# Kernel tuning notes

Hardware: AMD Instinct MI355X
Metric: run time of the kernel (lower is better)

Reference implementation:

```python
import jax, jax.numpy as jnp
import numpy as np


def setup_inputs() -> dict:
    key = jax.random.key(0)
    kq, kk, kv = jax.random.split(key, 3)
    B, H, T, D = 1, 16, 4096, 64
    Q = jax.random.normal(kq, (B, H, T, D), dtype=jnp.float32)
    K = jax.random.normal(kk, (B, H, T, D), dtype=jnp.float32)
    V = jax.random.normal(kv, (B, H, T, D), dtype=jnp.float32)
    return {"Q": Q, "K": K, "V": V}


def reference(Q, K, V):
    B, H, T, D = Q.shape
    # ALiBi slopes: m_h = 2^(-8*h/H), h = 1..H (deterministic buffer)
    slopes = jnp.exp2(-8.0 * jnp.arange(1, H + 1, dtype=jnp.float32) / H)
    pos = jnp.arange(T, dtype=jnp.float32)
    dist = jnp.abs(pos[None, :] - pos[:, None])          # (T, T)
    bias = slopes[:, None, None] * dist                   # (H, T, T)
    scale = jnp.sqrt(jnp.asarray(D, dtype=Q.dtype))
    scores = jnp.einsum('bhtd,bhsd->bhts', Q, K) / scale - bias[None]
    attn = jax.nn.softmax(scores, axis=-1)
    return jnp.einsum('bhts,bhsd->bhtd', attn, V)
```

## Files before the change

kernel.cpp:

```cpp
#include <hip/hip_runtime.h>
#include <hip/hip_bf16.h>
#include <stdint.h>

typedef float f4    __attribute__((ext_vector_type(4)));
typedef float f32x4 __attribute__((ext_vector_type(4)));
typedef short s16x8 __attribute__((ext_vector_type(8)));
typedef short s16x4 __attribute__((ext_vector_type(4)));
typedef unsigned short u16;

#define T_LEN 4096
#define NHEAD 16
#define DHEAD 64
#define KVBLK 64
#define NT    (T_LEN / KVBLK)

#if __has_builtin(__builtin_amdgcn_exp2f)
#define EXP2(x) __builtin_amdgcn_exp2f(x)
#else
#define EXP2(x) exp2f(x)
#endif

#define SLOT_F 4160
#define CONV_BYTES ((size_t)16777216)
#define SLOTS_BAL  2304
#define BAL_BYTES  (CONV_BYTES + (size_t)SLOTS_BAL * SLOT_F * 4u)

__device__ __constant__ int NCARR[8] = {2,3,4,4,5,6,6,6};
__device__ __constant__ int SBARR[8] = {0,128,320,576,832,1152,1536,1920};

__device__ __forceinline__ uint32_t pk2(float a, float b){
  uint32_t ua = __builtin_bit_cast(uint32_t, a) + 0x8000u;
  uint32_t ub = __builtin_bit_cast(uint32_t, b) + 0x8000u;
  return __builtin_amdgcn_perm(ub, ua, 0x07060302u);
}
__device__ __forceinline__ int swk(int r){ return (r ^ (r >> 3)) & 7; }
__device__ __forceinline__ int sw(int r){ return swk(r) << 3; }

__global__ __launch_bounds__(256)
void cvt_kv(const float* __restrict__ K, const float* __restrict__ V,
            u16* __restrict__ Kb, u16* __restrict__ VT){
  __shared__ u16 tile[64][66];
  if (blockIdx.x < 2048){
    const size_t i = ((size_t)blockIdx.x * 256 + threadIdx.x) * 8;
    f4 a = *(const f4*)(K + i);
    f4 b = *(const f4*)(K + i + 4);
    union { uint32_t w[4]; s16x8 v; } u;
    u.w[0] = pk2(a[0], a[1]); u.w[1] = pk2(a[2], a[3]);
    u.w[2] = pk2(b[0], b[1]); u.w[3] = pk2(b[2], b[3]);
    *(s16x8*)(Kb + i) = u.v;
  } else {
    const int vb = blockIdx.x - 2048;
    const int h  = vb >> 6;
    const int kt = vb & 63;
    const int t  = threadIdx.x;
    const float* Vh = V + ((size_t)h * T_LEN + kt * 64) * DHEAD;

    const int r = t >> 2, c = (t & 3) * 16;
    f4 x0 = *(const f4*)(Vh + r*64 + c);
    f4 x1 = *(const f4*)(Vh + r*64 + c + 4);
    f4 x2 = *(const f4*)(Vh + r*64 + c + 8);
    f4 x3 = *(const f4*)(Vh + r*64 + c + 12);
    uint32_t* tp = (uint32_t*)&tile[r][c];
    tp[0] = pk2(x0[0],x0[1]); tp[1] = pk2(x0[2],x0[3]);
    tp[2] = pk2(x1[0],x1[1]); tp[3] = pk2(x1[2],x1[3]);
    tp[4] = pk2(x2[0],x2[1]); tp[5] = pk2(x2[2],x2[3]);
    tp[6] = pk2(x3[0],x3[1]); tp[7] = pk2(x3[2],x3[3]);
    __syncthreads();

    const int d = t >> 2, ks = (t & 3) * 16;
    u16* op = VT + ((size_t)h * DHEAD + d) * T_LEN + kt * 64 + ks;
    union { uint32_t w[4]; s16x8 v; } o0, o1;
#pragma unroll
    for (int q = 0; q < 4; ++q)
      o0.w[q] = (uint32_t)tile[ks + 2*q][d]     | ((uint32_t)tile[ks + 2*q + 1][d] << 16);
#pragma unroll
    for (int q = 0; q < 4; ++q)
      o1.w[q] = (uint32_t)tile[ks + 8 + 2*q][d] | ((uint32_t)tile[ks + 9 + 2*q][d] << 16);
    *(s16x8*)(op)     = o0.v;
    *(s16x8*)(op + 8) = o1.v;
  }
}

__global__ __launch_bounds__(256, 4)
void alibi_attn5(const float* __restrict__ Qg,
                 const u16* __restrict__ Kb,
                 const u16* __restrict__ VTb,
                 float* __restrict__ Og,
                 float* __restrict__ part)
{
  __shared__ u16 kbuf[2][KVBLK * DHEAD];
  __shared__ u16 vbuf[2][DHEAD * KVBLK];

  int h, qt, c, n;
  {
    int r = blockIdx.x;
    if (r < 1152){
      h = 15 - r / 384; r %= 384; n = 6; qt = r / 6; c = r % 6;
    } else if ((r -= 1152) < 320){
      h = 12; n = 5; qt = r / 5; c = r % 5;
    } else if ((r -= 320) < 512){
      h = 11 - (r >> 8); r &= 255; n = 4; qt = r >> 2; c = r & 3;
    } else if ((r -= 512) < 192){
      h = 9; n = 3; qt = r / 3; c = r % 3;
    } else if ((r -= 192) < 128){
      h = 8; n = 2; qt = r >> 1; c = r & 1;
    } else {
      r -= 128; h = r >> 6; qt = r & 63; n = 1; c = 0;
    }
  }

  const int tid  = threadIdx.x;
  const int wv   = tid >> 6;
  const int lane = tid & 63;
  const int lg   = lane >> 4;
  const int ln   = lane & 15;

  const int q0   = qt * 64;
  const int qrow = q0 + wv * 16 + ln;
  const float slope = exp2f(-0.5f * (float)(h + 1));
  const float cs = 0.125f * 1.44269504089f;
  const float bs = slope * 1.44269504089f;
  const size_t headoff = (size_t)h * T_LEN * DHEAD;

  const int Di = (int)(36.0f / bs);
  int lo = (q0 - Di) >> 6;           if (lo < 0) lo = 0;
  int hi = (q0 + 63 + Di) >> 6;      if (hi > NT - 1) hi = NT - 1;
  const int len = hi - lo + 1;
  const int start = lo + (c * len) / n;
  const int end   = lo + ((c + 1) * len) / n;

  s16x8 qf0, qf1;
  {
    const float* qp = Qg + headoff + (size_t)qrow * DHEAD + lg * 8;
    f4 x = *(const f4*)qp;        f4 y = *(const f4*)(qp + 4);
    f4 z = *(const f4*)(qp + 32); f4 v = *(const f4*)(qp + 36);
    union { uint32_t w_[4]; s16x8 v_; } u0, u1;
    u0.w_[0] = pk2(x[0]*cs, x[1]*cs); u0.w_[1] = pk2(x[2]*cs, x[3]*cs);
    u0.w_[2] = pk2(y[0]*cs, y[1]*cs); u0.w_[3] = pk2(y[2]*cs, y[3]*cs);
    u1.w_[0] = pk2(z[0]*cs, z[1]*cs); u1.w_[1] = pk2(z[2]*cs, z[3]*cs);
    u1.w_[2] = pk2(v[0]*cs, v[1]*cs); u1.w_[3] = pk2(v[2]*cs, v[3]*cs);
    qf0 = u0.v_; qf1 = u1.v_;
  }

  f32x4 acc[4];
#pragma unroll
  for (int dt = 0; dt < 4; ++dt) acc[dt] = (f32x4)(0.0f);
  float lsum = 0.0f;
  const float base0 = (float)qrow - (float)(lg * 4);

  int koffs[4][2];
#pragma unroll
  for (int kt = 0; kt < 4; ++kt){
    const int key = kt*16 + ln, sz = sw(key);
    koffs[kt][0] = (((key*64      + lg*8) ^ sz)) * 2;
    koffs[kt][1] = (((key*64 + 32 + lg*8) ^ sz)) * 2;
  }
  int voffs[4][4];
#pragma unroll
  for (int dt = 0; dt < 4; ++dt){
    const int d = dt*16 + ln, sz = sw(d);
#pragma unroll
    for (int kt = 0; kt < 4; ++kt)
      voffs[dt][kt] = (((d*64 + kt*16 + lg*4) ^ sz)) * 2;
  }

  const u16* Kh = Kb  + headoff;
  const u16* Vh = VTb + headoff;
  const int sA = wv * 128 + lane;
  const int sB = sA + 64;
  const int keyA = sA >> 3, gA = (sA & 7) ^ swk(keyA);
  const int keyB = sB >> 3, gB = (sB & 7) ^ swk(keyB);
  const int kidxA = keyA * 64 + gA * 8;
  const int kidxB = keyB * 64 + gB * 8;
  const int vidxA = keyA * T_LEN + gA * 8;
  const int vidxB = keyB * T_LEN + gB * 8;
  const int dstA = sA * 16, dstB = sB * 16;

  s16x8 rkA, rkB, rvA, rvB;
  auto ldregs = [&](int t){
    const u16* kp = Kh + (size_t)t * (KVBLK * DHEAD);
    const u16* vp = Vh + (size_t)t * KVBLK;
    rkA = *(const s16x8*)(kp + kidxA);  rkB = *(const s16x8*)(kp + kidxB);
    rvA = *(const s16x8*)(vp + vidxA);  rvB = *(const s16x8*)(vp + vidxB);
  };
  auto wrregs = [&](u16* kb_, u16* vb_){
    *(s16x8*)((char*)kb_ + dstA) = rkA;  *(s16x8*)((char*)kb_ + dstB) = rkB;
    *(s16x8*)((char*)vb_ + dstA) = rvA;  *(s16x8*)((char*)vb_ + dstB) = rvB;
  };

  auto compute = [&](const u16* kb_, const u16* vb_, int kv){
    f32x4 S[4];
    __builtin_amdgcn_s_setprio(1);
#pragma unroll
    for (int kt = 0; kt < 4; ++kt){
      s16x8 k0 = *(const s16x8*)((const char*)kb_ + koffs[kt][0]);
      s16x8 k1 = *(const s16x8*)((const char*)kb_ + koffs[kt][1]);
      f32x4 cc = (f32x4)(0.0f);
      cc = __builtin_amdgcn_mfma_f32_16x16x32_bf16(k0, qf0, cc, 0, 0, 0);
      cc = __builtin_amdgcn_mfma_f32_16x16x32_bf16(k1, qf1, cc, 0, 0, 0);
      S[kt] = cc;
    }
    __builtin_amdgcn_s_setprio(0);

    const float bi = base0 - (float)(kv * KVBLK);
    float p[16];
#pragma unroll
    for (int kt = 0; kt < 4; ++kt)
#pragma unroll
      for (int r = 0; r < 4; ++r)
        p[kt*4 + r] = EXP2(fmaf(-bs, fabsf(bi - (float)(kt*16 + r)), S[kt][r]));

    lsum += (((p[0]+p[1]) + (p[2]+p[3])) + ((p[4]+p[5]) + (p[6]+p[7])))
          + (((p[8]+p[9]) + (p[10]+p[11])) + ((p[12]+p[13]) + (p[14]+p[15])));

    s16x4 pb[4];
#pragma unroll
    for (int kt = 0; kt < 4; ++kt){
      union { uint32_t w_[2]; s16x4 v_; } u;
      u.w_[0] = pk2(p[kt*4+0], p[kt*4+1]);
      u.w_[1] = pk2(p[kt*4+2], p[kt*4+3]);
      pb[kt] = u.v_;
    }

    __builtin_amdgcn_s_setprio(1);
#pragma unroll
    for (int dt = 0; dt < 4; ++dt){
#pragma unroll
      for (int kt = 0; kt < 4; ++kt){
        const s16x4 vf = *(const s16x4*)((const char*)vb_ + voffs[dt][kt]);
        acc[dt] = __builtin_amdgcn_mfma_f32_16x16x16bf16_1k(vf, pb[kt], acc[dt], 0, 0, 0);
      }
    }
    __builtin_amdgcn_s_setprio(0);
  };

  {
    ldregs(start);
    wrregs(kbuf[0], vbuf[0]);
    __syncthreads();

    const int hi_i = end - 1;
    int t = start;
#pragma unroll 1
    while (t + 1 < hi_i){
      ldregs(t + 1);
      compute(kbuf[0], vbuf[0], t);
      wrregs(kbuf[1], vbuf[1]);
      __syncthreads();
      ldregs(t + 2);
      compute(kbuf[1], vbuf[1], t + 1);
      wrregs(kbuf[0], vbuf[0]);
      __syncthreads();
      t += 2;
    }
    if (t < hi_i){
      ldregs(t + 1);
      compute(kbuf[0], vbuf[0], t);
      wrregs(kbuf[1], vbuf[1]);
      __syncthreads();
      compute(kbuf[1], vbuf[1], t + 1);
    } else {
      compute(kbuf[0], vbuf[0], t);
    }
  }

  lsum += __shfl_xor(lsum, 16, 64);
  lsum += __shfl_xor(lsum, 32, 64);

  if (n == 1){
    const float inv = 1.0f / lsum;
    float* op = Og + headoff + (size_t)qrow * DHEAD + lg * 4;
#pragma unroll
    for (int dt = 0; dt < 4; ++dt){
      f4 o;
      o[0] = acc[dt][0] * inv; o[1] = acc[dt][1] * inv;
      o[2] = acc[dt][2] * inv; o[3] = acc[dt][3] * inv;
      *(f4*)(op + dt*16) = o;
    }
  } else {
    float* slot = part + (size_t)(SBARR[h - 8] + qt * n + c) * SLOT_F;
    const int row = wv * 16 + ln;
    float* op = slot + row * 64 + lg * 4;
#pragma unroll
    for (int dt = 0; dt < 4; ++dt)
      *(f4*)(op + dt*16) = acc[dt];
    if (lg == 0) slot[4096 + row] = lsum;
  }
}

__global__ __launch_bounds__(256)
void combine_k(const float* __restrict__ part, float* __restrict__ Og){
  const int h  = 8 + (blockIdx.x >> 6);
  const int qt = blockIdx.x & 63;
  const int n  = NCARR[h - 8];
  const int sb = SBARR[h - 8] + qt * n;

  const int t   = threadIdx.x;
  const int row = t >> 2;
  const int seg = (t & 3) * 16;

  f4 a0 = (f4)(0.0f), a1 = (f4)(0.0f), a2 = (f4)(0.0f), a3 = (f4)(0.0f);
  float l = 0.0f;
#pragma unroll 1
  for (int c = 0; c < n; ++c){
    const float* sp = part + (size_t)(sb + c) * SLOT_F;
    const float* rp = sp + row * 64 + seg;
    a0 += *(const f4*)(rp);
    a1 += *(const f4*)(rp + 4);
    a2 += *(const f4*)(rp + 8);
    a3 += *(const f4*)(rp + 12);
    l  += sp[4096 + row];
  }
  const float inv = 1.0f / l;
  float* op = Og + (((size_t)h * T_LEN + qt * 64 + row) * DHEAD) + seg;
  f4 o0, o1, o2, o3;
  o0[0]=a0[0]*inv; o0[1]=a0[1]*inv; o0[2]=a0[2]*inv; o0[3]=a0[3]*inv;
  o1[0]=a1[0]*inv; o1[1]=a1[1]*inv; o1[2]=a1[2]*inv; o1[3]=a1[3]*inv;
  o2[0]=a2[0]*inv; o2[1]=a2[1]*inv; o2[2]=a2[2]*inv; o2[3]=a2[3]*inv;
  o3[0]=a3[0]*inv; o3[1]=a3[1]*inv; o3[2]=a3[2]*inv; o3[3]=a3[3]*inv;
  *(f4*)(op)      = o0;
  *(f4*)(op + 4)  = o1;
  *(f4*)(op + 8)  = o2;
  *(f4*)(op + 12) = o3;
}

__global__ __launch_bounds__(256, 4)
void alibi_attn4(const float* __restrict__ Qg,
                 const u16* __restrict__ Kb,
                 const u16* __restrict__ VTb,
                 float* __restrict__ Og)
{
  __shared__ u16 kbuf[2][KVBLK * DHEAD];
  __shared__ u16 vbuf[2][DHEAD * KVBLK];

  const int bid = blockIdx.x;
  const int fid = (bid & 7) * 128 + (bid >> 3);
  const int h  = fid & 15;
  const int qt = fid >> 4;

  const int tid  = threadIdx.x;
  const int wv   = tid >> 6;
  const int lane = tid & 63;
  const int lg   = lane >> 4;
  const int ln   = lane & 15;

  const int q0   = qt * 64;
  const int qrow = q0 + wv * 16 + ln;
  const float slope = exp2f(-0.5f * (float)(h + 1));
  const float cs = 0.125f * 1.44269504089f;
  const float bs = slope * 1.44269504089f;
  const size_t headoff = (size_t)h * T_LEN * DHEAD;

  const int Di = (int)(36.0f / bs);
  int lo = (q0 - Di) >> 6;           if (lo < 0) lo = 0;
  int hi = (q0 + 63 + Di) >> 6;      if (hi > NT - 1) hi = NT - 1;

  s16x8 qf0, qf1;
  {
    const float* qp = Qg + headoff + (size_t)qrow * DHEAD + lg * 8;
    f4 x = *(const f4*)qp;        f4 y = *(const f4*)(qp + 4);
    f4 z = *(const f4*)(qp + 32); f4 v = *(const f4*)(qp + 36);
    union { uint32_t w_[4]; s16x8 v_; } u0, u1;
    u0.w_[0] = pk2(x[0]*cs, x[1]*cs); u0.w_[1] = pk2(x[2]*cs, x[3]*cs);
    u0.w_[2] = pk2(y[0]*cs, y[1]*cs); u0.w_[3] = pk2(y[2]*cs, y[3]*cs);
    u1.w_[0] = pk2(z[0]*cs, z[1]*cs); u1.w_[1] = pk2(z[2]*cs, z[3]*cs);
    u1.w_[2] = pk2(v[0]*cs, v[1]*cs); u1.w_[3] = pk2(v[2]*cs, v[3]*cs);
    qf0 = u0.v_; qf1 = u1.v_;
  }

  f32x4 acc[4];
#pragma unroll
  for (int dt = 0; dt < 4; ++dt) acc[dt] = (f32x4)(0.0f);
  float lsum = 0.0f;
  const float base0 = (float)qrow - (float)(lg * 4);

  int koffs[4][2];
#pragma unroll
  for (int kt = 0; kt < 4; ++kt){
    const int key = kt*16 + ln, sz = sw(key);
    koffs[kt][0] = (((key*64      + lg*8) ^ sz)) * 2;
    koffs[kt][1] = (((key*64 + 32 + lg*8) ^ sz)) * 2;
  }
  int voffs[4][4];
#pragma unroll
  for (int dt = 0; dt < 4; ++dt){
    const int d = dt*16 + ln, sz = sw(d);
#pragma unroll
    for (int kt = 0; kt < 4; ++kt)
      voffs[dt][kt] = (((d*64 + kt*16 + lg*4) ^ sz)) * 2;
  }

  const u16* Kh = Kb  + headoff;
  const u16* Vh = VTb + headoff;
  const int sA = wv * 128 + lane;
  const int sB = sA + 64;
  const int keyA = sA >> 3, gA = (sA & 7) ^ swk(keyA);
  const int keyB = sB >> 3, gB = (sB & 7) ^ swk(keyB);
  const int kidxA = keyA * 64 + gA * 8;
  const int kidxB = keyB * 64 + gB * 8;
  const int vidxA = keyA * T_LEN + gA * 8;
  const int vidxB = keyB * T_LEN + gB * 8;
  const int dstA = sA * 16, dstB = sB * 16;

  s16x8 rkA, rkB, rvA, rvB;
  auto ldregs = [&](int t){
    const u16* kp = Kh + (size_t)t * (KVBLK * DHEAD);
    const u16* vp = Vh + (size_t)t * KVBLK;
    rkA = *(const s16x8*)(kp + kidxA);  rkB = *(const s16x8*)(kp + kidxB);
    rvA = *(const s16x8*)(vp + vidxA);  rvB = *(const s16x8*)(vp + vidxB);
  };
  auto wrregs = [&](u16* kb_, u16* vb_){
    *(s16x8*)((char*)kb_ + dstA) = rkA;  *(s16x8*)((char*)kb_ + dstB) = rkB;
    *(s16x8*)((char*)vb_ + dstA) = rvA;  *(s16x8*)((char*)vb_ + dstB) = rvB;
  };

  auto compute = [&](const u16* kb_, const u16* vb_, int kv){
    f32x4 S[4];
    __builtin_amdgcn_s_setprio(1);
#pragma unroll
    for (int kt = 0; kt < 4; ++kt){
      s16x8 k0 = *(const s16x8*)((const char*)kb_ + koffs[kt][0]);
      s16x8 k1 = *(const s16x8*)((const char*)kb_ + koffs[kt][1]);
      f32x4 cc = (f32x4)(0.0f);
      cc = __builtin_amdgcn_mfma_f32_16x16x32_bf16(k0, qf0, cc, 0, 0, 0);
      cc = __builtin_amdgcn_mfma_f32_16x16x32_bf16(k1, qf1, cc, 0, 0, 0);
      S[kt] = cc;
    }
    __builtin_amdgcn_s_setprio(0);

    const float bi = base0 - (float)(kv * KVBLK);
    float p[16];
#pragma unroll
    for (int kt = 0; kt < 4; ++kt)
#pragma unroll
      for (int r = 0; r < 4; ++r)
        p[kt*4 + r] = EXP2(fmaf(-bs, fabsf(bi - (float)(kt*16 + r)), S[kt][r]));

    lsum += (((p[0]+p[1]) + (p[2]+p[3])) + ((p[4]+p[5]) + (p[6]+p[7])))
          + (((p[8]+p[9]) + (p[10]+p[11])) + ((p[12]+p[13]) + (p[14]+p[15])));

    s16x4 pb[4];
#pragma unroll
    for (int kt = 0; kt < 4; ++kt){
      union { uint32_t w_[2]; s16x4 v_; } u;
      u.w_[0] = pk2(p[kt*4+0], p[kt*4+1]);
      u.w_[1] = pk2(p[kt*4+2], p[kt*4+3]);
      pb[kt] = u.v_;
    }

    __builtin_amdgcn_s_setprio(1);
#pragma unroll
    for (int dt = 0; dt < 4; ++dt){
#pragma unroll
      for (int kt = 0; kt < 4; ++kt){
        const s16x4 vf = *(const s16x4*)((const char*)vb_ + voffs[dt][kt]);
        acc[dt] = __builtin_amdgcn_mfma_f32_16x16x16bf16_1k(vf, pb[kt], acc[dt], 0, 0, 0);
      }
    }
    __builtin_amdgcn_s_setprio(0);
  };

  ldregs(lo);
  wrregs(kbuf[0], vbuf[0]);
  __syncthreads();

  int t = lo;
#pragma unroll 1
  while (t + 1 < hi){
    ldregs(t + 1);
    compute(kbuf[0], vbuf[0], t);
    wrregs(kbuf[1], vbuf[1]);
    __syncthreads();
    ldregs(t + 2);
    compute(kbuf[1], vbuf[1], t + 1);
    wrregs(kbuf[0], vbuf[0]);
    __syncthreads();
    t += 2;
  }
  if (t < hi){
    ldregs(t + 1);
    compute(kbuf[0], vbuf[0], t);
    wrregs(kbuf[1], vbuf[1]);
    __syncthreads();
    compute(kbuf[1], vbuf[1], t + 1);
  } else {
    compute(kbuf[0], vbuf[0], t);
  }

  lsum += __shfl_xor(lsum, 16, 64);
  lsum += __shfl_xor(lsum, 32, 64);
  const float inv = 1.0f / lsum;
  float* op = Og + headoff + (size_t)qrow * DHEAD + lg * 4;
#pragma unroll
  for (int dt = 0; dt < 4; ++dt){
    f4 o;
    o[0] = acc[dt][0] * inv; o[1] = acc[dt][1] * inv;
    o[2] = acc[dt][2] * inv; o[3] = acc[dt][3] * inv;
    *(f4*)(op + dt*16) = o;
  }
}

__global__ __launch_bounds__(256, 2)
void alibi_attn_fb(const float* __restrict__ Qg,
                   const float* __restrict__ Kg,
                   const float* __restrict__ Vg,
                   float* __restrict__ Og)
{
  __shared__ u16 kbuf[2][KVBLK * DHEAD];
  __shared__ u16 vbuf[2][DHEAD * KVBLK];

  const int bid = blockIdx.x;
  const int fid = (bid & 7) * 64 + (bid >> 3);
  const int h  = fid >> 5;
  const int qt = fid & 31;

  const int tid  = threadIdx.x;
  const int wave = tid >> 6;
  const int lane = tid & 63;
  const int lg   = lane >> 4;
  const int ln   = lane & 15;

  const int qb = qt * 128 + wave * 32;
  const float slope = exp2f(-0.5f * (float)(h + 1));
  const float cs = 0.125f * 1.44269504089f;
  const float bs = slope * 1.44269504089f;
  const size_t headoff = (size_t)h * T_LEN * DHEAD;

  s16x8 qf[2][2];
#pragma unroll
  for (int rg = 0; rg < 2; ++rg)
#pragma unroll
    for (int dh = 0; dh < 2; ++dh){
      const float* qp = Qg + headoff + (size_t)(qb + rg*16 + ln) * DHEAD + dh*32 + lg*8;
      f4 x = *(const f4*)qp;
      f4 y = *(const f4*)(qp + 4);
      union { uint32_t w[4]; s16x8 v; } u;
      u.w[0] = pk2(x[0]*cs, x[1]*cs);
      u.w[1] = pk2(x[2]*cs, x[3]*cs);
      u.w[2] = pk2(y[0]*cs, y[1]*cs);
      u.w[3] = pk2(y[2]*cs, y[3]*cs);
      qf[rg][dh] = u.v;
    }

  f32x4 acc[2][4];
#pragma unroll
  for (int rg = 0; rg < 2; ++rg)
#pragma unroll
    for (int dt = 0; dt < 4; ++dt) acc[rg][dt] = (f32x4)(0.0f);
  float mreg[2] = {-1e30f, -1e30f};
  float lreg[2] = {0.0f, 0.0f};
  const float qposf[2] = {(float)(qb + ln), (float)(qb + 16 + ln)};
  const float koffb = (float)(lg * 4);

  f4 st4[8];
  const int vk0  = (tid >> 2) * 2;
  const int vseg = (tid & 3) * 16;
  const int krow = (tid - 128) >> 1;
  const int kseg = ((tid - 128) & 1) * 32;
  const float* Vb = Vg + headoff;
  const float* Kb_ = Kg + headoff;

  auto stage_load = [&](int kv){
    const int kb = kv * KVBLK;
    if (tid < 128){
      const float* vp = Vb + (size_t)(kb + vk0) * DHEAD + vseg;
      st4[0] = *(const f4*)(vp);      st4[1] = *(const f4*)(vp + 4);
      st4[2] = *(const f4*)(vp + 8);  st4[3] = *(const f4*)(vp + 12);
      st4[4] = *(const f4*)(vp + 64); st4[5] = *(const f4*)(vp + 68);
      st4[6] = *(const f4*)(vp + 72); st4[7] = *(const f4*)(vp + 76);
    } else {
      const float* kp = Kb_ + (size_t)(kb + krow) * DHEAD + kseg;
#pragma unroll
      for (int j = 0; j < 8; ++j) st4[j] = *(const f4*)(kp + j*4);
    }
  };
  auto stage_store = [&](int b){
    if (tid < 128){
#pragma unroll
      for (int i = 0; i < 16; ++i){
        const int d = vseg + i;
        uint32_t pr = pk2(st4[i>>2][i&3], st4[4 + (i>>2)][i&3]);
        *(uint32_t*)&vbuf[b][(d*64 + vk0) ^ sw(d)] = pr;
      }
    } else {
#pragma unroll
      for (int i = 0; i < 4; ++i){
        union { uint32_t w[4]; s16x8 v; } u;
        u.w[0] = pk2(st4[i*2][0],   st4[i*2][1]);
        u.w[1] = pk2(st4[i*2][2],   st4[i*2][3]);
        u.w[2] = pk2(st4[i*2+1][0], st4[i*2+1][1]);
        u.w[3] = pk2(st4[i*2+1][2], st4[i*2+1][3]);
        *(s16x8*)&kbuf[b][(krow*64 + kseg + i*8) ^ sw(krow)] = u.v;
      }
    }
  };

  stage_load(0);
  stage_store(0);
  __syncthreads();
  int cur = 0;

#pragma unroll 1
  for (int kv = 0; kv < NT; ++kv){
    if (kv + 1 < NT) stage_load(kv + 1);

    const float kbf = (float)(kv * KVBLK);
    const u16* kb_ = kbuf[cur];
    const u16* vb_ = vbuf[cur];

    s16x8 kf[4][2];
#pragma unroll
    for (int kt = 0; kt < 4; ++kt){
      const int key = kt*16 + ln;
      const int sz  = sw(key);
      kf[kt][0] = *(const s16x8*)&kb_[(key*64 +      lg*8) ^ sz];
      kf[kt][1] = *(const s16x8*)&kb_[(key*64 + 32 + lg*8) ^ sz];
    }
    f32x4 S[2][4];
#pragma unroll
    for (int rg = 0; rg < 2; ++rg)
#pragma unroll
      for (int kt = 0; kt < 4; ++kt){
        f32x4 c = (f32x4)(0.0f);
        c = __builtin_amdgcn_mfma_f32_16x16x32_bf16(kf[kt][0], qf[rg][0], c, 0, 0, 0);
        c = __builtin_amdgcn_mfma_f32_16x16x32_bf16(kf[kt][1], qf[rg][1], c, 0, 0, 0);
        S[rg][kt] = c;
      }

    s16x4 pb[2][4];
#pragma unroll
    for (int rg = 0; rg < 2; ++rg){
      const float base = qposf[rg] - kbf - koffb;
#pragma unroll
      for (int kt = 0; kt < 4; ++kt)
#pragma unroll
        for (int r = 0; r < 4; ++r)
          S[rg][kt][r] = fmaf(-bs, fabsf(base - (float)(kt*16 + r)), S[rg][kt][r]);

      float a0 = fmaxf(fmaxf(S[rg][0][0], S[rg][0][1]), fmaxf(S[rg][0][2], S[rg][0][3]));
      float a1 = fmaxf(fmaxf(S[rg][1][0], S[rg][1][1]), fmaxf(S[rg][1][2], S[rg][1][3]));
      float a2 = fmaxf(fmaxf(S[rg][2][0], S[rg][2][1]), fmaxf(S[rg][2][2], S[rg][2][3]));
      float a3 = fmaxf(fmaxf(S[rg][3][0], S[rg][3][1]), fmaxf(S[rg][3][2], S[rg][3][3]));
      float mx = fmaxf(fmaxf(a0, a1), fmaxf(a2, a3));
      mx = fmaxf(mx, __shfl_xor(mx, 16, 64));
      mx = fmaxf(mx, __shfl_xor(mx, 32, 64));

      const float mo = mreg[rg];
      const float mn = fmaxf(mo, mx);
      const float scl = EXP2(mo - mn);
      mreg[rg] = mn;

      float p[16];
#pragma unroll
      for (int kt = 0; kt < 4; ++kt)
#pragma unroll
        for (int r = 0; r < 4; ++r)
          p[kt*4 + r] = EXP2(S[rg][kt][r] - mn);

      float s0 = (p[0]+p[1]) + (p[2]+p[3]);
      float s1 = (p[4]+p[5]) + (p[6]+p[7]);
      float s2 = (p[8]+p[9]) + (p[10]+p[11]);
      float s3 = (p[12]+p[13]) + (p[14]+p[15]);
      float sum = (s0+s1) + (s2+s3);
      sum += __shfl_xor(sum, 16, 64);
      sum += __shfl_xor(sum, 32, 64);
      lreg[rg] = lreg[rg] * scl + sum;

#pragma unroll
      for (int dt = 0; dt < 4; ++dt) acc[rg][dt] *= scl;

#pragma unroll
      for (int kt = 0; kt < 4; ++kt){
        union { uint32_t w[2]; s16x4 v; } u;
        u.w[0] = pk2(p[kt*4+0], p[kt*4+1]);
        u.w[1] = pk2(p[kt*4+2], p[kt*4+3]);
        pb[rg][kt] = u.v;
      }
    }

#pragma unroll
    for (int dt = 0; dt < 4; ++dt){
      const int d  = dt*16 + ln;
      const int sz = sw(d);
#pragma unroll
      for (int kt = 0; kt < 4; ++kt){
        const s16x4 vf = *(const s16x4*)&vb_[(d*64 + kt*16 + lg*4) ^ sz];
        acc[0][dt] = __builtin_amdgcn_mfma_f32_16x16x16bf16_1k(vf, pb[0][kt], acc[0][dt], 0, 0, 0);
        acc[1][dt] = __builtin_amdgcn_mfma_f32_16x16x16bf16_1k(vf, pb[1][kt], acc[1][dt], 0, 0, 0);
      }
    }

    if (kv + 1 < NT){
      stage_store(cur ^ 1);
      __syncthreads();
      cur ^= 1;
    }
  }

#pragma unroll
  for (int rg = 0; rg < 2; ++rg){
    const float inv = 1.0f / lreg[rg];
    float* op = Og + headoff + (size_t)(qb + rg*16 + ln) * DHEAD + lg*4;
#pragma unroll
    for (int dt = 0; dt < 4; ++dt){
      f4 o;
      o[0] = acc[rg][dt][0] * inv;
      o[1] = acc[rg][dt][1] * inv;
      o[2] = acc[rg][dt][2] * inv;
      o[3] = acc[rg][dt][3] * inv;
      *(f4*)(op + dt*16) = o;
    }
  }
}

extern "C" void kernel_launch(void* const* d_in, const int* in_sizes, int n_in,
                              void* d_out, int out_size, void* d_ws, size_t ws_size,
                              hipStream_t stream)
{
  const float* Q = (const float*)d_in[0];
  const float* K = (const float*)d_in[1];
  const float* V = (const float*)d_in[2];
  float* O = (float*)d_out;

  if (ws_size >= BAL_BYTES){
    u16* Kb = (u16*)d_ws;
    u16* VT = Kb + (size_t)NHEAD * T_LEN * DHEAD;
    float* part = (float*)((char*)d_ws + CONV_BYTES);
    hipLaunchKernelGGL(cvt_kv, dim3(3072), dim3(256), 0, stream, K, V, Kb, VT);
    hipLaunchKernelGGL(alibi_attn5, dim3(2816), dim3(256), 0, stream, Q, Kb, VT, O, part);
    hipLaunchKernelGGL(combine_k, dim3(512), dim3(256), 0, stream, part, O);
  } else if (ws_size >= CONV_BYTES){
    u16* Kb = (u16*)d_ws;
    u16* VT = Kb + (size_t)NHEAD * T_LEN * DHEAD;
    hipLaunchKernelGGL(cvt_kv, dim3(3072), dim3(256), 0, stream, K, V, Kb, VT);
    hipLaunchKernelGGL(alibi_attn4, dim3(1024), dim3(256), 0, stream, Q, Kb, VT, O);
  } else {
    hipLaunchKernelGGL(alibi_attn_fb, dim3(512), dim3(256), 0, stream, Q, K, V, O);
  }
}
```

Measured before the change: 85.77 us.

## Double query tile to 128 rows with 512-thread blocks sharing each KV tile

The attention kernel now uses 512-thread blocks (8 waves) covering 128 query rows, so each staged K/V tile in shared memory is reused by twice as many query rows. Each thread now loads one 16-byte chunk per tile instead of two. The split-KV work distribution is rebalanced per head (new chunk counts and slot offsets), and the combine kernel is reshaped for 128-row tiles. This halves block count and per-row K/V staging traffic. The cost is wider KV ranges per block under the ALiBi window, and lower occupancy granularity per CU.

```diff
diff --git a/kernel.cpp b/kernel.cpp
--- a/kernel.cpp
+++ b/kernel.cpp
@@ -20,13 +20,13 @@
 #define EXP2(x) exp2f(x)
 #endif
 
-#define SLOT_F 4160
+#define SLOT_F 8320
 #define CONV_BYTES ((size_t)16777216)
-#define SLOTS_BAL  2304
+#define SLOTS_BAL  1152
 #define BAL_BYTES  (CONV_BYTES + (size_t)SLOTS_BAL * SLOT_F * 4u)
 
-__device__ __constant__ int NCARR[8] = {2,3,4,4,5,6,6,6};
-__device__ __constant__ int SBARR[8] = {0,128,320,576,832,1152,1536,1920};
+__device__ __constant__ int NCARR[8] = {2,2,3,5,6,6,6,6};
+__device__ __constant__ int SBARR[8] = {1088,1024,928,768,576,384,192,0};
 
 __device__ __forceinline__ uint32_t pk2(float a, float b){
   uint32_t ua = __builtin_bit_cast(uint32_t, a) + 0x8000u;
@@ -81,8 +81,8 @@
   }
 }
 
-__global__ __launch_bounds__(256, 4)
-void alibi_attn5(const float* __restrict__ Qg,
+__global__ __launch_bounds__(512, 4)
+void alibi_attn7(const float* __restrict__ Qg,
                  const u16* __restrict__ Kb,
                  const u16* __restrict__ VTb,
                  float* __restrict__ Og,
@@ -91,21 +91,21 @@
   __shared__ u16 kbuf[2][KVBLK * DHEAD];
   __shared__ u16 vbuf[2][DHEAD * KVBLK];
 
-  int h, qt, c, n;
+  int h, qt, c, n, sb;
   {
     int r = blockIdx.x;
-    if (r < 1152){
-      h = 15 - r / 384; r %= 384; n = 6; qt = r / 6; c = r % 6;
-    } else if ((r -= 1152) < 320){
-      h = 12; n = 5; qt = r / 5; c = r % 5;
-    } else if ((r -= 320) < 512){
-      h = 11 - (r >> 8); r &= 255; n = 4; qt = r >> 2; c = r & 3;
-    } else if ((r -= 512) < 192){
-      h = 9; n = 3; qt = r / 3; c = r % 3;
-    } else if ((r -= 192) < 128){
-      h = 8; n = 2; qt = r >> 1; c = r & 1;
+    if (r < 768){
+      h = 15 - r / 192; r %= 192; n = 6; qt = r / 6; c = r % 6; sb = (15 - h) * 192;
+    } else if ((r -= 768) < 160){
+      h = 11; n = 5; qt = r / 5; c = r % 5; sb = 768;
+    } else if ((r -= 160) < 96){
+      h = 10; n = 3; qt = r / 3; c = r % 3; sb = 928;
+    } else if ((r -= 96) < 64){
+      h = 9; n = 2; qt = r >> 1; c = r & 1; sb = 1024;
+    } else if ((r -= 64) < 64){
+      h = 8; n = 2; qt = r >> 1; c = r & 1; sb = 1088;
     } else {
-      r -= 128; h = r >> 6; qt = r & 63; n = 1; c = 0;
+      r -= 64; h = r >> 5; qt = r & 31; n = 1; c = 0; sb = 0;
     }
   }
 
@@ -115,7 +115,7 @@
   const int lg   = lane >> 4;
   const int ln   = lane & 15;
 
-  const int q0   = qt * 64;
+  const int q0   = qt * 128;
   const int qrow = q0 + wv * 16 + ln;
   const float slope = exp2f(-0.5f * (float)(h + 1));
   const float cs = 0.125f * 1.44269504089f;
@@ -124,7 +124,7 @@
 
   const int Di = (int)(36.0f / bs);
   int lo = (q0 - Di) >> 6;           if (lo < 0) lo = 0;
-  int hi = (q0 + 63 + Di) >> 6;      if (hi > NT - 1) hi = NT - 1;
+  int hi = (q0 + 127 + Di) >> 6;     if (hi > NT - 1) hi = NT - 1;
   const int len = hi - lo + 1;
   const int start = lo + (c * len) / n;
   const int end   = lo + ((c + 1) * len) / n;
@@ -166,26 +166,19 @@
 
   const u16* Kh = Kb  + headoff;
   const u16* Vh = VTb + headoff;
-  const int sA = wv * 128 + lane;
-  const int sB = sA + 64;
-  const int keyA = sA >> 3, gA = (sA & 7) ^ swk(keyA);
-  const int keyB = sB >> 3, gB = (sB & 7) ^ swk(keyB);
+  const int keyA = tid >> 3, gA = (tid & 7) ^ swk(keyA);
   const int kidxA = keyA * 64 + gA * 8;
-  const int kidxB = keyB * 64 + gB * 8;
   const int vidxA = keyA * T_LEN + gA * 8;
-  const int vidxB = keyB * T_LEN + gB * 8;
-  const int dstA = sA * 16, dstB = sB * 16;
-
-  s16x8 rkA, rkB, rvA, rvB;
+  const int dstA = tid * 16;
+
+  s16x8 rkA, rvA;
   auto ldregs = [&](int t){
-    const u16* kp = Kh + (size_t)t * (KVBLK * DHEAD);
-    const u16* vp = Vh + (size_t)t * KVBLK;
-    rkA = *(const s16x8*)(kp + kidxA);  rkB = *(const s16x8*)(kp + kidxB);
-    rvA = *(const s16x8*)(vp + vidxA);  rvB = *(const s16x8*)(vp + vidxB);
+    rkA = *(const s16x8*)(Kh + (size_t)t * (KVBLK * DHEAD) + kidxA);
+    rvA = *(const s16x8*)(Vh + (size_t)t * KVBLK + vidxA);
   };
   auto wrregs = [&](u16* kb_, u16* vb_){
-    *(s16x8*)((char*)kb_ + dstA) = rkA;  *(s16x8*)((char*)kb_ + dstB) = rkB;
-    *(s16x8*)((char*)vb_ + dstA) = rvA;  *(s16x8*)((char*)vb_ + dstB) = rvB;
+    *(s16x8*)((char*)kb_ + dstA) = rkA;
+    *(s16x8*)((char*)vb_ + dstA) = rvA;
   };
 
   auto compute = [&](const u16* kb_, const u16* vb_, int kv){
@@ -278,50 +271,47 @@
       *(f4*)(op + dt*16) = o;
     }
   } else {
-    float* slot = part + (size_t)(SBARR[h - 8] + qt * n + c) * SLOT_F;
+    float* slot = part + (size_t)(sb + qt * n + c) * SLOT_F;
     const int row = wv * 16 + ln;
     float* op = slot + row * 64 + lg * 4;
 #pragma unroll
     for (int dt = 0; dt < 4; ++dt)
       *(f4*)(op + dt*16) = acc[dt];
-    if (lg == 0) slot[4096 + row] = lsum;
+    if (lg == 0) slot[8192 + row] = lsum;
   }
 }
 
 __global__ __launch_bounds__(256)
 void combine_k(const float* __restrict__ part, float* __restrict__ Og){
-  const int h  = 8 + (blockIdx.x >> 6);
-  const int qt = blockIdx.x & 63;
+  const int h  = 8 + (blockIdx.x >> 5);
+  const int qt = blockIdx.x & 31;
   const int n  = NCARR[h - 8];
   const int sb = SBARR[h - 8] + qt * n;
 
   const int t   = threadIdx.x;
-  const int row = t >> 2;
-  const int seg = (t & 3) * 16;
-
-  f4 a0 = (f4)(0.0f), a1 = (f4)(0.0f), a2 = (f4)(0.0f), a3 = (f4)(0.0f);
+  const int row = t >> 1;
+  const int seg = (t & 1) * 32;
+
+  f4 a[8];
+#pragma unroll
+  for (int i = 0; i < 8; ++i) a[i] = (f4)(0.0f);
   float l = 0.0f;
 #pragma unroll 1
   for (int c = 0; c < n; ++c){
     const float* sp = part + (size_t)(sb + c) * SLOT_F;
     const float* rp = sp + row * 64 + seg;
-    a0 += *(const f4*)(rp);
-    a1 += *(const f4*)(rp + 4);
-    a2 += *(const f4*)(rp + 8);
-    a3 += *(const f4*)(rp + 12);
-    l  += sp[4096 + row];
+#pragma unroll
+    for (int i = 0; i < 8; ++i) a[i] += *(const f4*)(rp + i*4);
+    l += sp[8192 + row];
   }
   const float inv = 1.0f / l;
-  float* op = Og + (((size_t)h * T_LEN + qt * 64 + row) * DHEAD) + seg;
-  f4 o0, o1, o2, o3;
-  o0[0]=a0[0]*inv; o0[1]=a0[1]*inv; o0[2]=a0[2]*inv; o0[3]=a0[3]*inv;
-  o1[0]=a1[0]*inv; o1[1]=a1[1]*inv; o1[2]=a1[2]*inv; o1[3]=a1[3]*inv;
-  o2[0]=a2[0]*inv; o2[1]=a2[1]*inv; o2[2]=a2[2]*inv; o2[3]=a2[3]*inv;
-  o3[0]=a3[0]*inv; o3[1]=a3[1]*inv; o3[2]=a3[2]*inv; o3[3]=a3[3]*inv;
-  *(f4*)(op)      = o0;
-  *(f4*)(op + 4)  = o1;
-  *(f4*)(op + 8)  = o2;
-  *(f4*)(op + 12) = o3;
+  float* op = Og + (((size_t)h * T_LEN + qt * 128 + row) * DHEAD) + seg;
+#pragma unroll
+  for (int i = 0; i < 8; ++i){
+    f4 o;
+    o[0] = a[i][0]*inv; o[1] = a[i][1]*inv; o[2] = a[i][2]*inv; o[3] = a[i][3]*inv;
+    *(f4*)(op + i*4) = o;
+  }
 }
 
 __global__ __launch_bounds__(256, 4)
@@ -727,8 +717,8 @@
     u16* VT = Kb + (size_t)NHEAD * T_LEN * DHEAD;
     float* part = (float*)((char*)d_ws + CONV_BYTES);
     hipLaunchKernelGGL(cvt_kv, dim3(3072), dim3(256), 0, stream, K, V, Kb, VT);
-    hipLaunchKernelGGL(alibi_attn5, dim3(2816), dim3(256), 0, stream, Q, Kb, VT, O, part);
-    hipLaunchKernelGGL(combine_k, dim3(512), dim3(256), 0, stream, part, O);
+    hipLaunchKernelGGL(alibi_attn7, dim3(1408), dim3(512), 0, stream, Q, Kb, VT, O, part);
+    hipLaunchKernelGGL(combine_k, dim3(256), dim3(256), 0, stream, part, O);
   } else if (ws_size >= CONV_BYTES){
     u16* Kb = (u16*)d_ws;
     u16* VT = Kb + (size_t)NHEAD * T_LEN * DHEAD;
```

Result: slower. 88.50 us (+3.2%).
